# Kernel tuning notes

Measured on AMD Instinct MI355X. Metric: run time of the kernel, lower is better.

## Reference

```python
import jax, jax.numpy as jnp
import numpy as np

B, T, C = 4, 2048, 1024
NUM_HEADS, HEAD_DIM = 16, 64
INNER = NUM_HEADS * HEAD_DIM
OUT_DIM = 1024


def setup_inputs() -> dict:
    key = jax.random.key(0)
    kx, kk, kq, kv, kp = jax.random.split(key, 5)
    return {
        "x": jax.random.normal(kx, (B, T, C), dtype=jnp.float32),
        "W_k": jax.random.normal(kk, (INNER, C), dtype=jnp.float32),
        "W_q": jax.random.normal(kq, (INNER, C), dtype=jnp.float32),
        "W_v": jax.random.normal(kv, (INNER, C), dtype=jnp.float32),
        "W_p": jax.random.normal(kp, (OUT_DIM, INNER), dtype=jnp.float32),
    }


def reference(x, W_k, W_q, W_v, W_p):
    b, t, c = x.shape
    h, d = NUM_HEADS, HEAD_DIM
    scale_in = c ** (-0.5)
    # project and split heads: [B, H, T, D]
    def proj(W):
        y = jnp.einsum('btc,ic->bti', x, W) * scale_in
        return y.reshape(b, t, h, d).transpose(0, 2, 1, 3)
    k = proj(W_k)
    q = proj(W_q)
    v = proj(W_v)
    scores = jnp.einsum('bhqd,bhkd->bhqk', q, k) * (d ** (-0.5))
    weight = jax.nn.softmax(scores, axis=-1)
    out = jnp.einsum('bhqk,bhkd->bhqd', weight, v)  # [B,H,T,D]
    out = out.transpose(0, 2, 1, 3).reshape(b, t, h * d)
    out = jnp.einsum('bti,oi->bto', out, W_p) * (W_p.shape[-1] ** (-0.5))
    return out
```

## Files before the change

kernel.cpp:

```cpp
#include <hip/hip_runtime.h>
#include <math.h>

typedef __attribute__((ext_vector_type(8))) short bh8;
typedef __attribute__((ext_vector_type(4))) float f32x4;

namespace {
constexpr int Bn = 4, Tn = 2048, Cn = 1024, Hn = 16, Dn = 64, INNERn = 1024, OUTn = 1024;
constexpr int Mn = Bn * Tn;
}

__device__ __forceinline__ void glds16(const void* g, void* l) {
    __builtin_amdgcn_global_load_lds(
        (const __attribute__((address_space(1))) void*)g,
        (__attribute__((address_space(3))) void*)l, 16, 0, 0);
}

__device__ __forceinline__ void barrier_vm0() {
    __builtin_amdgcn_s_waitcnt(0x0070);
    __builtin_amdgcn_s_barrier();
}

__device__ __forceinline__ ushort f2bf(float f) {
    union { float f; unsigned u; } v; v.f = f;
    unsigned r = v.u + 0x7fffu + ((v.u >> 16) & 1u);
    return (ushort)(r >> 16);
}
__device__ __forceinline__ unsigned pack_rne(float a, float b) {
    return (unsigned)f2bf(a) | ((unsigned)f2bf(b) << 16);
}
__device__ __forceinline__ unsigned pack_trunc(float a, float b) {
    return __builtin_amdgcn_perm(__float_as_uint(a), __float_as_uint(b), 0x03020706u);
}

__global__ __launch_bounds__(256)
void cvt_all(const float* __restrict__ x,  const float* __restrict__ Wk,
             const float* __restrict__ Wq, const float* __restrict__ Wv,
             const float* __restrict__ Wp,
             ushort* __restrict__ xb,  ushort* __restrict__ wkb,
             ushort* __restrict__ wqb, ushort* __restrict__ wvb,
             ushort* __restrict__ wpb)
{
    const int bid = blockIdx.x;
    const float* s; ushort* d; float sc; int i;
    if (bid < 8192) {
        s = x; d = xb; sc = 0.03125f;
        i = bid * 256 + threadIdx.x;
    } else {
        const int seg = (bid - 8192) >> 10;
        i = ((bid - 8192) & 1023) * 256 + threadIdx.x;
        s  = (seg == 0) ? Wk : (seg == 1) ? Wq : (seg == 2) ? Wv : Wp;
        d  = (seg == 0) ? wkb : (seg == 1) ? wqb : (seg == 2) ? wvb : wpb;
        sc = (seg == 3) ? 0.03125f : 1.0f;
    }
    float4 f = ((const float4*)s)[i];
    ushort4 o;
    o.x = f2bf(f.x * sc); o.y = f2bf(f.y * sc);
    o.z = f2bf(f.z * sc); o.w = f2bf(f.w * sc);
    ((ushort4*)d)[i] = o;
}

__global__ __launch_bounds__(256)
void gemm_qkv(const ushort* __restrict__ A, const ushort* __restrict__ Wq,
              const ushort* __restrict__ Wk, const ushort* __restrict__ Wv,
              ushort* __restrict__ Oq, ushort* __restrict__ Ok,
              ushort* __restrict__ Ovt, float qscale)
{
    __shared__ char As[2][8192];
    __shared__ char Bs[2][8192];
    const int tid = threadIdx.x;
    const int w = tid >> 6, lane = tid & 63, quad = lane >> 4, l = lane & 15;
    const int sel = blockIdx.x >> 3;
    const ushort* Bw = (sel == 0) ? Wq : (sel == 1) ? Wk : Wv;
    const int n0 = (blockIdx.x & 7) * 128, m0 = blockIdx.y * 128;
    const int wm = w >> 1, wn = w & 1;

    auto stage = [&](int bsel, int k0) {
#pragma unroll
        for (int rr = 0; rr < 2; ++rr) {
            const int rho = w * 2 + rr;
            const int row = rho * 16 + (lane >> 2);
            const int kq  = (lane & 3) * 8;
            glds16(A  + (size_t)(m0 + row) * Cn + k0 + kq, As[bsel] + rho * 1024 + lane * 16);
            glds16(Bw + (size_t)(n0 + row) * Cn + k0 + kq, Bs[bsel] + rho * 1024 + lane * 16);
        }
    };

    f32x4 acc[4][4];
#pragma unroll
    for (int i = 0; i < 4; ++i)
#pragma unroll
        for (int j = 0; j < 4; ++j) acc[i][j] = (f32x4){0.f, 0.f, 0.f, 0.f};

    stage(0, 0);
    barrier_vm0();
#pragma unroll 2
    for (int it = 0; it < 32; ++it) {
        const int cur = it & 1;
        if (it < 31) stage(cur ^ 1, (it + 1) * 32);
        const char* Ac = As[cur]; const char* Bc = Bs[cur];
        bh8 af[4], bf[4];
#pragma unroll
        for (int mf = 0; mf < 4; ++mf)
            af[mf] = *(const bh8*)(Ac + (wm * 64 + mf * 16 + l) * 64 + quad * 16);
#pragma unroll
        for (int nf = 0; nf < 4; ++nf)
            bf[nf] = *(const bh8*)(Bc + (wn * 64 + nf * 16 + l) * 64 + quad * 16);
#pragma unroll
        for (int mf = 0; mf < 4; ++mf)
#pragma unroll
            for (int nf = 0; nf < 4; ++nf)
                acc[mf][nf] = __builtin_amdgcn_mfma_f32_16x16x32_bf16(af[mf], bf[nf], acc[mf][nf], 0, 0, 0);
        barrier_vm0();
    }

    if (sel < 2) {
        ushort* dU = (sel == 0) ? Oq : Ok;
        const float scale = (sel == 0) ? qscale : 1.0f;
#pragma unroll
        for (int mf = 0; mf < 4; ++mf)
#pragma unroll
            for (int nf = 0; nf < 4; ++nf) {
                const int mb = m0 + wm * 64 + mf * 16 + quad * 4;
                const int n  = n0 + wn * 64 + nf * 16 + l;
                const int h = n >> 6, dd = n & 63;
#pragma unroll
                for (int reg = 0; reg < 4; ++reg) {
                    const int m = mb + reg;
                    const int b = m >> 11, t = m & (Tn - 1);
                    dU[((size_t)(b * Hn + h) * Tn + t) * Dn + dd] = f2bf(acc[mf][nf][reg]* scale);
                }
            }
    } else {
#pragma unroll
        for (int mf = 0; mf < 4; ++mf)
#pragma unroll
            for (int nf = 0; nf < 4; ++nf) {
                const int mb = m0 + wm * 64 + mf * 16 + quad * 4;
                const int n  = n0 + wn * 64 + nf * 16 + l;
                const int h = n >> 6, dd = n & 63;
                const int b = mb >> 11, t0 = mb & (Tn - 1);
                uint2 p;
                p.x = pack_rne(acc[mf][nf][0], acc[mf][nf][1]);
                p.y = pack_rne(acc[mf][nf][2], acc[mf][nf][3]);
                *(uint2*)(Ovt + ((size_t)(b * Hn + h) * Dn + dd) * Tn + t0) = p;
            }
    }
}

__global__ __launch_bounds__(256)
void gemm_po(const ushort* __restrict__ A, const ushort* __restrict__ Bw,
             float* __restrict__ Cout)
{
    __shared__ char As[2][8192];
    __shared__ char Bs[2][8192];
    const int tid = threadIdx.x;
    const int w = tid >> 6, lane = tid & 63, quad = lane >> 4, l = lane & 15;
    const int n0 = blockIdx.x * 128, m0 = blockIdx.y * 128;
    const int wm = w >> 1, wn = w & 1;

    auto stage = [&](int bsel, int k0) {
#pragma unroll
        for (int rr = 0; rr < 2; ++rr) {
            const int rho = w * 2 + rr;
            const int row = rho * 16 + (lane >> 2);
            const int kq  = (lane & 3) * 8;
            glds16(A  + (size_t)(m0 + row) * Cn + k0 + kq, As[bsel] + rho * 1024 + lane * 16);
            glds16(Bw + (size_t)(n0 + row) * Cn + k0 + kq, Bs[bsel] + rho * 1024 + lane * 16);
        }
    };

    f32x4 acc[4][4];
#pragma unroll
    for (int i = 0; i < 4; ++i)
#pragma unroll
        for (int j = 0; j < 4; ++j) acc[i][j] = (f32x4){0.f, 0.f, 0.f, 0.f};

    stage(0, 0);
    barrier_vm0();
#pragma unroll 2
    for (int it = 0; it < 32; ++it) {
        const int cur = it & 1;
        if (it < 31) stage(cur ^ 1, (it + 1) * 32);
        const char* Ac = As[cur]; const char* Bc = Bs[cur];
        bh8 af[4], bf[4];
#pragma unroll
        for (int mf = 0; mf < 4; ++mf)
            af[mf] = *(const bh8*)(Ac + (wm * 64 + mf * 16 + l) * 64 + quad * 16);
#pragma unroll
        for (int nf = 0; nf < 4; ++nf)
            bf[nf] = *(const bh8*)(Bc + (wn * 64 + nf * 16 + l) * 64 + quad * 16);
#pragma unroll
        for (int mf = 0; mf < 4; ++mf)
#pragma unroll
            for (int nf = 0; nf < 4; ++nf)
                acc[mf][nf] = __builtin_amdgcn_mfma_f32_16x16x32_bf16(af[mf], bf[nf], acc[mf][nf], 0, 0, 0);
        barrier_vm0();
    }

#pragma unroll
    for (int mf = 0; mf < 4; ++mf)
#pragma unroll
        for (int nf = 0; nf < 4; ++nf) {
            const int mb = m0 + wm * 64 + mf * 16 + quad * 4;
            const int n  = n0 + wn * 64 + nf * 16 + l;
#pragma unroll
            for (int reg = 0; reg < 4; ++reg)
                Cout[(size_t)(mb + reg) * OUTn + n] = acc[mf][nf][reg];
        }
}

__global__ __launch_bounds__(256, 3)
void attn_mfma(const ushort* __restrict__ Qg, const ushort* __restrict__ Kg,
               const ushort* __restrict__ Vtg, ushort* __restrict__ Og)
{
    __shared__ char KT[2][8192];
    __shared__ char VT[2][8192];
    __shared__ char PS[16384];

    const int tid = threadIdx.x;
    const int w = tid >> 6, lane = tid & 63, quad = lane >> 4, l = lane & 15;
    const int q0 = blockIdx.x * 128;
    const int bh = blockIdx.y, b = bh >> 4, h = bh & 15;
    const ushort* Qp = Qg  + (size_t)bh * Tn * Dn;
    const ushort* Kp = Kg  + (size_t)bh * Tn * Dn;
    const ushort* Vp = Vtg + (size_t)bh * Dn * Tn;

    auto stageK = [&](char* buf, int kt) {
#pragma unroll
        for (int rr = 0; rr < 2; ++rr) {
            const int rho = w * 2 + rr;
            const int r  = (rho & 3) * 16 + (lane >> 2);
            const int dq = (rho >> 2) * 32 + (lane & 3) * 8;
            glds16(Kp + (size_t)(kt * 64 + r) * Dn + dq, buf + rho * 1024 + lane * 16);
        }
    };
    auto stageV = [&](char* buf, int kt) {
#pragma unroll
        for (int rr = 0; rr < 2; ++rr) {
            const int rho = w * 2 + rr;
            const int d = rho * 8 + (lane >> 3);
            const int csrc = (lane & 7) ^ ((lane >> 3) & 7);
            glds16(Vp + (size_t)d * Tn + kt * 64 + csrc * 8, buf + rho * 1024 + lane * 16);
        }
    };

    bh8 qf[2][2];
#pragma unroll
    for (int nt = 0; nt < 2; ++nt)
#pragma unroll
        for (int ks = 0; ks < 2; ++ks)
            qf[nt][ks] = *(const bh8*)(Qp + (size_t)(q0 + w * 32 + nt * 16 + l) * Dn + ks * 32 + quad * 8);

    bh8 ones;
#pragma unroll
    for (int i = 0; i < 8; ++i) ones[i] = (short)0x3F80;

    f32x4 oacc[2][4], lacc[2];
#pragma unroll
    for (int nt = 0; nt < 2; ++nt) {
        lacc[nt] = (f32x4){0.f, 0.f, 0.f, 0.f};
#pragma unroll
        for (int dt = 0; dt < 4; ++dt) oacc[nt][dt] = (f32x4){0.f, 0.f, 0.f, 0.f};
    }

    char* Pw = PS + w * 4096;
    const f32x4 zero = (f32x4){0.f, 0.f, 0.f, 0.f};

    stageK(KT[0], 0);
    stageV(VT[0], 0);
    barrier_vm0();

#pragma unroll 2
    for (int kt = 0; kt < Tn / 64; ++kt) {
        const int cur = kt & 1;
        if (kt < Tn / 64 - 1) {
            stageK(KT[cur ^ 1], kt + 1);
            stageV(VT[cur ^ 1], kt + 1);
        }
        const char* Kc = KT[cur];
        const char* Vc = VT[cur];

        f32x4 st[2][4];
#pragma unroll
        for (int k8 = 0; k8 < 4; ++k8) {
            bh8 kf = *(const bh8*)(Kc + (k8 * 16 + l) * 64 + quad * 16);
            st[0][k8] = __builtin_amdgcn_mfma_f32_16x16x32_bf16(kf, qf[0][0], zero, 0, 0, 0);
            st[1][k8] = __builtin_amdgcn_mfma_f32_16x16x32_bf16(kf, qf[1][0], zero, 0, 0, 0);
        }
#pragma unroll
        for (int k8 = 0; k8 < 4; ++k8) {
            bh8 kf = *(const bh8*)(Kc + 4096 + (k8 * 16 + l) * 64 + quad * 16);
            st[0][k8] = __builtin_amdgcn_mfma_f32_16x16x32_bf16(kf, qf[0][1], st[0][k8], 0, 0, 0);
            st[1][k8] = __builtin_amdgcn_mfma_f32_16x16x32_bf16(kf, qf[1][1], st[1][k8], 0, 0, 0);
        }

#pragma unroll
        for (int nt = 0; nt < 2; ++nt)
#pragma unroll
            for (int k8 = 0; k8 < 4; ++k8) {
                const float e0 = __builtin_amdgcn_exp2f(st[nt][k8][0]);
                const float e1 = __builtin_amdgcn_exp2f(st[nt][k8][1]);
                const float e2 = __builtin_amdgcn_exp2f(st[nt][k8][2]);
                const float e3 = __builtin_amdgcn_exp2f(st[nt][k8][3]);
                uint2 p;
                p.x = pack_trunc(e0, e1);
                p.y = pack_trunc(e2, e3);
                const int x = (k8 * 2 + (quad >> 1)) ^ (l & 7);
                *(uint2*)(Pw + (nt * 16 + l) * 128 + x * 16 + (quad & 1) * 8) = p;
            }
        __builtin_amdgcn_s_waitcnt(0xC07F);

#pragma unroll
        for (int cg = 0; cg < 2; ++cg) {
            const int xc = ((cg * 4 + quad) ^ (l & 7)) * 16;
            bh8 pf0 = *(const bh8*)(Pw + (0 * 16 + l) * 128 + xc);
            bh8 pf1 = *(const bh8*)(Pw + (1 * 16 + l) * 128 + xc);
            lacc[0] = __builtin_amdgcn_mfma_f32_16x16x32_bf16(ones, pf0, lacc[0], 0, 0, 0);
            lacc[1] = __builtin_amdgcn_mfma_f32_16x16x32_bf16(ones, pf1, lacc[1], 0, 0, 0);
#pragma unroll
            for (int dt = 0; dt < 4; ++dt) {
                bh8 vf = *(const bh8*)(Vc + (dt * 16 + l) * 128 + xc);
                oacc[0][dt] = __builtin_amdgcn_mfma_f32_16x16x32_bf16(vf, pf0, oacc[0][dt], 0, 0, 0);
                oacc[1][dt] = __builtin_amdgcn_mfma_f32_16x16x32_bf16(vf, pf1, oacc[1][dt], 0, 0, 0);
            }
        }
        barrier_vm0();
    }

#pragma unroll
    for (int nt = 0; nt < 2; ++nt) {
        const float inv = 1.0f / lacc[nt][0];
        const int t = q0 + w * 32 + nt * 16 + l;
#pragma unroll
        for (int dt = 0; dt < 4; ++dt) {
            uint2 p;
            p.x = pack_rne(oacc[nt][dt][0] * inv, oacc[nt][dt][1] * inv);
            p.y = pack_rne(oacc[nt][dt][2] * inv, oacc[nt][dt][3] * inv);
            *(uint2*)(Og + ((size_t)(b * Tn + t)) * INNERn + h * 64 + dt * 16 + quad * 4) = p;
        }
    }
}

extern "C" void kernel_launch(void* const* d_in, const int* in_sizes, int n_in,
                              void* d_out, int out_size, void* d_ws, size_t ws_size,
                              hipStream_t stream)
{
    const float* x  = (const float*)d_in[0];
    const float* Wk = (const float*)d_in[1];
    const float* Wq = (const float*)d_in[2];
    const float* Wv = (const float*)d_in[3];
    const float* Wp = (const float*)d_in[4];
    float* out = (float*)d_out;

    ushort* xb  = (ushort*)d_ws;
    ushort* wkb = xb  + (size_t)Mn * Cn;
    ushort* wqb = wkb + (size_t)INNERn * Cn;
    ushort* wvb = wqb + (size_t)INNERn * Cn;
    ushort* wpb = wvb + (size_t)INNERn * Cn;
    ushort* qw  = wpb + (size_t)OUTn * INNERn;
    ushort* kw  = qw  + (size_t)Mn * INNERn;
    ushort* vtw = kw  + (size_t)Mn * INNERn;
    ushort* aow = vtw + (size_t)Mn * INNERn;

    const dim3 blk(256);
    cvt_all<<<dim3(8192 + 4096), blk, 0, stream>>>(x, Wk, Wq, Wv, Wp,
                                                   xb, wkb, wqb, wvb, wpb);

    gemm_qkv<<<dim3(3 * 8, Mn / 128), blk, 0, stream>>>(xb, wqb, wkb, wvb,
                                                        qw, kw, vtw, 0.125f * 1.44269504f);

    attn_mfma<<<dim3(Tn / 128, Bn * Hn), blk, 0, stream>>>(qw, kw, vtw, aow);

    gemm_po<<<dim3(OUTn / 128, Mn / 128), blk, 0, stream>>>(aow, wpb, out);
}
```

Before: 287.2 us.

## Double attention query tile per block to reuse K/V tiles across more rows

Each attention block now handles 256 query rows (64 per wave) instead of 128, so every staged K/V tile feeds twice as many MFMAs. The inner loop is split into two 32-key halves so the per-wave P scratch still fits in 4 KB. Launch bounds drop to 2 blocks per CU and the unroll pragma is removed to make room for the extra accumulators. In exchange the grid is halved to 512 blocks and register pressure rises, which can lower occupancy and reduce how well loads are hidden.

```diff
diff --git a/kernel.cpp b/kernel.cpp
--- a/kernel.cpp
+++ b/kernel.cpp
@@ -127,7 +127,7 @@
                 for (int reg = 0; reg < 4; ++reg) {
                     const int m = mb + reg;
                     const int b = m >> 11, t = m & (Tn - 1);
-                    dU[((size_t)(b * Hn + h) * Tn + t) * Dn + dd] = f2bf(acc[mf][nf][reg]* scale);
+                    dU[((size_t)(b * Hn + h) * Tn + t) * Dn + dd] = f2bf(acc[mf][nf][reg] * scale);
                 }
             }
     } else {
@@ -209,7 +209,7 @@
         }
 }
 
-__global__ __launch_bounds__(256, 3)
+__global__ __launch_bounds__(256, 2)
 void attn_mfma(const ushort* __restrict__ Qg, const ushort* __restrict__ Kg,
                const ushort* __restrict__ Vtg, ushort* __restrict__ Og)
 {
@@ -219,7 +219,7 @@
 
     const int tid = threadIdx.x;
     const int w = tid >> 6, lane = tid & 63, quad = lane >> 4, l = lane & 15;
-    const int q0 = blockIdx.x * 128;
+    const int q0 = blockIdx.x * 256;
     const int bh = blockIdx.y, b = bh >> 4, h = bh & 15;
     const ushort* Qp = Qg  + (size_t)bh * Tn * Dn;
     const ushort* Kp = Kg  + (size_t)bh * Tn * Dn;
@@ -244,20 +244,20 @@
         }
     };
 
-    bh8 qf[2][2];
-#pragma unroll
-    for (int nt = 0; nt < 2; ++nt)
+    bh8 qf[4][2];
+#pragma unroll
+    for (int nt = 0; nt < 4; ++nt)
 #pragma unroll
         for (int ks = 0; ks < 2; ++ks)
-            qf[nt][ks] = *(const bh8*)(Qp + (size_t)(q0 + w * 32 + nt * 16 + l) * Dn + ks * 32 + quad * 8);
+            qf[nt][ks] = *(const bh8*)(Qp + (size_t)(q0 + w * 64 + nt * 16 + l) * Dn + ks * 32 + quad * 8);
 
     bh8 ones;
 #pragma unroll
     for (int i = 0; i < 8; ++i) ones[i] = (short)0x3F80;
 
-    f32x4 oacc[2][4], lacc[2];
-#pragma unroll
-    for (int nt = 0; nt < 2; ++nt) {
+    f32x4 oacc[4][4], lacc[4];
+#pragma unroll
+    for (int nt = 0; nt < 4; ++nt) {
         lacc[nt] = (f32x4){0.f, 0.f, 0.f, 0.f};
 #pragma unroll
         for (int dt = 0; dt < 4; ++dt) oacc[nt][dt] = (f32x4){0.f, 0.f, 0.f, 0.f};
@@ -270,7 +270,6 @@
     stageV(VT[0], 0);
     barrier_vm0();
 
-#pragma unroll 2
     for (int kt = 0; kt < Tn / 64; ++kt) {
         const int cur = kt & 1;
         if (kt < Tn / 64 - 1) {
@@ -280,57 +279,62 @@
         const char* Kc = KT[cur];
         const char* Vc = VT[cur];
 
-        f32x4 st[2][4];
-#pragma unroll
-        for (int k8 = 0; k8 < 4; ++k8) {
-            bh8 kf = *(const bh8*)(Kc + (k8 * 16 + l) * 64 + quad * 16);
-            st[0][k8] = __builtin_amdgcn_mfma_f32_16x16x32_bf16(kf, qf[0][0], zero, 0, 0, 0);
-            st[1][k8] = __builtin_amdgcn_mfma_f32_16x16x32_bf16(kf, qf[1][0], zero, 0, 0, 0);
-        }
-#pragma unroll
-        for (int k8 = 0; k8 < 4; ++k8) {
-            bh8 kf = *(const bh8*)(Kc + 4096 + (k8 * 16 + l) * 64 + quad * 16);
-            st[0][k8] = __builtin_amdgcn_mfma_f32_16x16x32_bf16(kf, qf[0][1], st[0][k8], 0, 0, 0);
-            st[1][k8] = __builtin_amdgcn_mfma_f32_16x16x32_bf16(kf, qf[1][1], st[1][k8], 0, 0, 0);
-        }
-
-#pragma unroll
-        for (int nt = 0; nt < 2; ++nt)
-#pragma unroll
-            for (int k8 = 0; k8 < 4; ++k8) {
-                const float e0 = __builtin_amdgcn_exp2f(st[nt][k8][0]);
-                const float e1 = __builtin_amdgcn_exp2f(st[nt][k8][1]);
-                const float e2 = __builtin_amdgcn_exp2f(st[nt][k8][2]);
-                const float e3 = __builtin_amdgcn_exp2f(st[nt][k8][3]);
-                uint2 p;
-                p.x = pack_trunc(e0, e1);
-                p.y = pack_trunc(e2, e3);
-                const int x = (k8 * 2 + (quad >> 1)) ^ (l & 7);
-                *(uint2*)(Pw + (nt * 16 + l) * 128 + x * 16 + (quad & 1) * 8) = p;
+#pragma unroll
+        for (int hh = 0; hh < 2; ++hh) {
+            bh8 kf[2][2];
+#pragma unroll
+            for (int k8l = 0; k8l < 2; ++k8l)
+#pragma unroll
+                for (int ks = 0; ks < 2; ++ks)
+                    kf[k8l][ks] = *(const bh8*)(Kc + ks * 4096 + ((hh * 2 + k8l) * 16 + l) * 64 + quad * 16);
+
+            f32x4 st[4][2];
+#pragma unroll
+            for (int nt = 0; nt < 4; ++nt)
+#pragma unroll
+                for (int k8l = 0; k8l < 2; ++k8l) {
+                    st[nt][k8l] = __builtin_amdgcn_mfma_f32_16x16x32_bf16(kf[k8l][0], qf[nt][0], zero, 0, 0, 0);
+                    st[nt][k8l] = __builtin_amdgcn_mfma_f32_16x16x32_bf16(kf[k8l][1], qf[nt][1], st[nt][k8l], 0, 0, 0);
+                }
+
+#pragma unroll
+            for (int nt = 0; nt < 4; ++nt)
+#pragma unroll
+                for (int k8l = 0; k8l < 2; ++k8l) {
+                    const float e0 = __builtin_amdgcn_exp2f(st[nt][k8l][0]);
+                    const float e1 = __builtin_amdgcn_exp2f(st[nt][k8l][1]);
+                    const float e2 = __builtin_amdgcn_exp2f(st[nt][k8l][2]);
+                    const float e3 = __builtin_amdgcn_exp2f(st[nt][k8l][3]);
+                    uint2 p;
+                    p.x = pack_trunc(e0, e1);
+                    p.y = pack_trunc(e2, e3);
+                    const int x = (k8l * 2 + (quad >> 1)) ^ (l & 3);
+                    *(uint2*)(Pw + (nt * 16 + l) * 64 + x * 16 + (quad & 1) * 8) = p;
+                }
+            __builtin_amdgcn_s_waitcnt(0xC07F);
+
+            bh8 pf[4];
+#pragma unroll
+            for (int nt = 0; nt < 4; ++nt)
+                pf[nt] = *(const bh8*)(Pw + (nt * 16 + l) * 64 + ((quad ^ (l & 3)) * 16));
+#pragma unroll
+            for (int nt = 0; nt < 4; ++nt)
+                lacc[nt] = __builtin_amdgcn_mfma_f32_16x16x32_bf16(ones, pf[nt], lacc[nt], 0, 0, 0);
+#pragma unroll
+            for (int dt = 0; dt < 4; ++dt) {
+                bh8 vf = *(const bh8*)(Vc + (dt * 16 + l) * 128 + (((hh * 4 + quad) ^ (l & 7)) * 16));
+#pragma unroll
+                for (int nt = 0; nt < 4; ++nt)
+                    oacc[nt][dt] = __builtin_amdgcn_mfma_f32_16x16x32_bf16(vf, pf[nt], oacc[nt][dt], 0, 0, 0);
             }
-        __builtin_amdgcn_s_waitcnt(0xC07F);
-
-#pragma unroll
-        for (int cg = 0; cg < 2; ++cg) {
-            const int xc = ((cg * 4 + quad) ^ (l & 7)) * 16;
-            bh8 pf0 = *(const bh8*)(Pw + (0 * 16 + l) * 128 + xc);
-            bh8 pf1 = *(const bh8*)(Pw + (1 * 16 + l) * 128 + xc);
-            lacc[0] = __builtin_amdgcn_mfma_f32_16x16x32_bf16(ones, pf0, lacc[0], 0, 0, 0);
-            lacc[1] = __builtin_amdgcn_mfma_f32_16x16x32_bf16(ones, pf1, lacc[1], 0, 0, 0);
-#pragma unroll
-            for (int dt = 0; dt < 4; ++dt) {
-                bh8 vf = *(const bh8*)(Vc + (dt * 16 + l) * 128 + xc);
-                oacc[0][dt] = __builtin_amdgcn_mfma_f32_16x16x32_bf16(vf, pf0, oacc[0][dt], 0, 0, 0);
-                oacc[1][dt] = __builtin_amdgcn_mfma_f32_16x16x32_bf16(vf, pf1, oacc[1][dt], 0, 0, 0);
-            }
         }
         barrier_vm0();
     }
 
 #pragma unroll
-    for (int nt = 0; nt < 2; ++nt) {
+    for (int nt = 0; nt < 4; ++nt) {
         const float inv = 1.0f / lacc[nt][0];
-        const int t = q0 + w * 32 + nt * 16 + l;
+        const int t = q0 + w * 64 + nt * 16 + l;
 #pragma unroll
         for (int dt = 0; dt < 4; ++dt) {
             uint2 p;
@@ -369,7 +373,7 @@
     gemm_qkv<<<dim3(3 * 8, Mn / 128), blk, 0, stream>>>(xb, wqb, wkb, wvb,
                                                         qw, kw, vtw, 0.125f * 1.44269504f);
 
-    attn_mfma<<<dim3(Tn / 128, Bn * Hn), blk, 0, stream>>>(qw, kw, vtw, aow);
+    attn_mfma<<<dim3(Tn / 256, Bn * Hn), blk, 0, stream>>>(qw, kw, vtw, aow);
 
     gemm_po<<<dim3(OUTn / 128, Mn / 128), blk, 0, stream>>>(aow, wpb, out);
 }
```

Result: no change. 290.8 us (+1.2%).
